# Performance work log

Hardware: AMD Instinct MI355X
Metric: run time of the kernel (lower is better)

Reference implementation:

```python
import jax, jax.numpy as jnp
import numpy as np

DIM = 512
HEADS = 8
DHEAD = DIM // 8          # 64
INNER = HEADS * DHEAD     # 512
M = DIM // 2              # 256 landmarks
ITERS = 6                 # pinv iterations
SCALE = DHEAD ** -0.5
LN_EPS = 1e-5             # torch LayerNorm default
KCONV = 33                # residual_conv_kernel default


def setup_inputs() -> dict:
    key = jax.random.key(0)
    ks = jax.random.split(key, 5)
    B, N = 2, 4096
    x = jax.random.normal(ks[0], (B, N, DIM), jnp.float32)
    ln_w = jnp.ones((DIM,), jnp.float32)
    ln_b = jnp.zeros((DIM,), jnp.float32)
    qkv_w = jax.random.normal(ks[1], (3 * INNER, DIM), jnp.float32) * 0.02
    out_w = jax.random.normal(ks[2], (DIM, INNER), jnp.float32) * 0.02
    out_b = jnp.zeros((DIM,), jnp.float32)
    conv_w = jax.random.normal(ks[3], (HEADS, 1, KCONV, 1), jnp.float32) * 0.05
    return dict(x=x, ln_w=ln_w, ln_b=ln_b, qkv_w=qkv_w,
                out_w=out_w, out_b=out_b, conv_w=conv_w)


def moore_penrose_pinv(x, iters=ITERS):
    # faithful to lucidrains: global (scalar) max over row/col abs-sums
    abs_x = jnp.abs(x)
    z = jnp.swapaxes(x, -1, -2) / (jnp.max(abs_x.sum(-1)) * jnp.max(abs_x.sum(-2)))
    I = jnp.eye(x.shape[-1], dtype=x.dtype)
    for _ in range(iters):
        xz = x @ z
        z = 0.25 * z @ (13 * I - xz @ (15 * I - xz @ (7 * I - xz)))
    return z


def reference(x, ln_w, ln_b, qkv_w, out_w, out_b, conv_w):
    B, N, D = x.shape
    # LayerNorm
    mu = x.mean(-1, keepdims=True)
    var = ((x - mu) ** 2).mean(-1, keepdims=True)
    xn = (x - mu) / jnp.sqrt(var + LN_EPS) * ln_w + ln_b
    # qkv projection (N divisible by M -> no padding branch)
    qkv = xn @ qkv_w.T                                   # [B,N,3*INNER]
    q, k, v = jnp.split(qkv, 3, axis=-1)

    def to_heads(t):
        return t.reshape(B, N, HEADS, DHEAD).transpose(0, 2, 1, 3)  # [B,H,N,Dh]

    q, k, v = to_heads(q), to_heads(k), to_heads(v)
    q = q * SCALE
    l = N // M  # tokens per landmark
    q_land = q.reshape(B, HEADS, M, l, DHEAD).mean(3)    # [B,H,M,Dh]
    k_land = k.reshape(B, HEADS, M, l, DHEAD).mean(3)
    sim1 = jnp.einsum('bhid,bhjd->bhij', q, k_land)      # [B,H,N,M]
    sim2 = jnp.einsum('bhid,bhjd->bhij', q_land, k_land) # [B,H,M,M]
    sim3 = jnp.einsum('bhid,bhjd->bhij', q_land, k)      # [B,H,M,N]
    a1 = jax.nn.softmax(sim1, -1)
    a2 = jax.nn.softmax(sim2, -1)
    a3 = jax.nn.softmax(sim3, -1)
    a2_inv = moore_penrose_pinv(a2)
    out = (a1 @ a2_inv) @ (a3 @ v)                       # [B,H,N,Dh]
    # depthwise residual conv on v along sequence (kernel 33, pad 16)
    res = jax.lax.conv_general_dilated(
        v, conv_w, window_strides=(1, 1),
        padding=((KCONV // 2, KCONV // 2), (0, 0)),
        dimension_numbers=('NCHW', 'OIHW', 'NCHW'),
        feature_group_count=HEADS)
    out = out + res
    out = out.transpose(0, 2, 1, 3).reshape(B, N, INNER)
    attn_out = out @ out_w.T + out_b                     # dropout = eval identity
    return x + attn_out
```

## Files before the change

kernel.cpp:

```cpp
#include <hip/hip_runtime.h>
#include <math.h>

#define DIMD  512
#define NSEQ  4096
#define BATCH 2
#define HEADS 8
#define DHEAD 64
#define MLAND 256
#define BH    (BATCH*HEADS)
#define QSCALE 0.125f
#define LN_EPS 1e-5f
#define KCONV 33

typedef __attribute__((ext_vector_type(8))) short bf16x8;
typedef __attribute__((ext_vector_type(4))) float f32x4;

#define WB(p, mb) ((char*)(p) + (size_t)(mb) * 1048576ull)

__device__ __forceinline__ unsigned short f2b(float f) {
  unsigned u = __float_as_uint(f);
  return (unsigned short)((u + 0x7FFFu + ((u >> 16) & 1u)) >> 16);
}
__device__ __forceinline__ float b2f(unsigned short h) {
  return __uint_as_float(((unsigned)h) << 16);
}

__device__ __forceinline__ float block_red(float v, float* s4, bool sum) {
#pragma unroll
  for (int o = 32; o; o >>= 1) {
    float t = __shfl_xor(v, o);
    v = sum ? v + t : fmaxf(v, t);
  }
  int wid = threadIdx.x >> 6;
  if ((threadIdx.x & 63) == 0) s4[wid] = v;
  __syncthreads();
  float r = sum ? (s4[0] + s4[1] + s4[2] + s4[3])
                : fmaxf(fmaxf(s4[0], s4[1]), fmaxf(s4[2], s4[3]));
  __syncthreads();
  return r;
}

__device__ __forceinline__ void gload16(const unsigned short* g, short* lds) {
  __builtin_amdgcn_global_load_lds(
      (const __attribute__((address_space(1))) void*)g,
      (__attribute__((address_space(3))) void*)lds, 16, 0, 0);
}

template<int ROWS>
__device__ __forceinline__ void stage_lds(const unsigned short* __restrict__ g, int ld,
                                          short* lds, int tid) {
  int l = tid & 63, w = tid >> 6;
  int r_in = l >> 2, c8 = (l & 3) * 8;
  constexpr int PER = ROWS / 64;
#pragma unroll
  for (int p = 0; p < PER; ++p) {
    int r0 = (w * PER + p) * 16;
    gload16(g + (size_t)(r0 + r_in) * ld + c8, lds + r0 * 32);
  }
}

__device__ __forceinline__ void mma_step32(const short* As, const short* Bs,
                                           int wrow, int wcol, int l, f32x4 acc[4][4]) {
  int lr = l & 15, lk = (l >> 4) * 8;
  bf16x8 af[4], bf_[4];
#pragma unroll
  for (int f = 0; f < 4; ++f) {
    af[f]  = *(const bf16x8*)&As[(wrow + f * 16 + lr) * 32 + lk];
    bf_[f] = *(const bf16x8*)&Bs[(wcol + f * 16 + lr) * 32 + lk];
  }
#pragma unroll
  for (int i = 0; i < 4; ++i)
#pragma unroll
    for (int j = 0; j < 4; ++j)
      acc[i][j] = __builtin_amdgcn_mfma_f32_16x16x32_bf16(af[i], bf_[j], acc[i][j], 0, 0, 0);
}


__global__ void k_init(unsigned* scal) {
  if (threadIdx.x < 4) scal[threadIdx.x] = 0u;
}

__global__ __launch_bounds__(256) void k_ln(const float* __restrict__ x,
                                            const float* __restrict__ w,
                                            const float* __restrict__ b,
                                            unsigned short* __restrict__ xnh) {
  int lane = threadIdx.x & 63;
  int row = blockIdx.x * 4 + (threadIdx.x >> 6);
  const float* xr = x + (size_t)row * DIMD;
  float4 v0 = *(const float4*)&xr[lane * 8];
  float4 v1 = *(const float4*)&xr[lane * 8 + 4];
  float s  = v0.x + v0.y + v0.z + v0.w + v1.x + v1.y + v1.z + v1.w;
  float ss = v0.x*v0.x + v0.y*v0.y + v0.z*v0.z + v0.w*v0.w
           + v1.x*v1.x + v1.y*v1.y + v1.z*v1.z + v1.w*v1.w;
#pragma unroll
  for (int o = 32; o; o >>= 1) { s += __shfl_xor(s, o); ss += __shfl_xor(ss, o); }
  float mu = s * (1.f / 512.f);
  float var = ss * (1.f / 512.f) - mu * mu;
  float rstd = rsqrtf(var + LN_EPS);
  float4 w0 = *(const float4*)&w[lane * 8];
  float4 w1 = *(const float4*)&w[lane * 8 + 4];
  float4 b0 = *(const float4*)&b[lane * 8];
  float4 b1 = *(const float4*)&b[lane * 8 + 4];
  float o0x = (v0.x - mu) * rstd * w0.x + b0.x;
  float o0y = (v0.y - mu) * rstd * w0.y + b0.y;
  float o0z = (v0.z - mu) * rstd * w0.z + b0.z;
  float o0w = (v0.w - mu) * rstd * w0.w + b0.w;
  float o1x = (v1.x - mu) * rstd * w1.x + b1.x;
  float o1y = (v1.y - mu) * rstd * w1.y + b1.y;
  float o1z = (v1.z - mu) * rstd * w1.z + b1.z;
  float o1w = (v1.w - mu) * rstd * w1.w + b1.w;
  uint4 pk;
  pk.x = (unsigned)f2b(o0x) | ((unsigned)f2b(o0y) << 16);
  pk.y = (unsigned)f2b(o0z) | ((unsigned)f2b(o0w) << 16);
  pk.z = (unsigned)f2b(o1x) | ((unsigned)f2b(o1y) << 16);
  pk.w = (unsigned)f2b(o1z) | ((unsigned)f2b(o1w) << 16);
  *(uint4*)&xnh[(size_t)row * DIMD + lane * 8] = pk;
}

__global__ __launch_bounds__(256) void k_wconv(const float* __restrict__ qkvw,
                                               const float* __restrict__ outw,
                                               unsigned short* __restrict__ wqh,
                                               unsigned short* __restrict__ owh) {
  int idx = blockIdx.x * 256 + threadIdx.x;
  if (idx < 786432) wqh[idx] = f2b(qkvw[idx]);
  else owh[idx - 786432] = f2b(outw[idx - 786432]);
}

__global__ __launch_bounds__(256) void k_qkv_mfma(const unsigned short* __restrict__ xnh,
                                                  const unsigned short* __restrict__ wqh,
                                                  unsigned short* __restrict__ qh,
                                                  unsigned short* __restrict__ kh,
                                                  unsigned short* __restrict__ vh,
                                                  unsigned short* __restrict__ vTh) {
  __shared__ short As[128 * 32], Bs[128 * 32];
  int tid = threadIdx.x, l = tid & 63, wid = tid >> 6;
  int wrow = (wid >> 1) * 64, wcol = (wid & 1) * 64;
  int m0 = blockIdx.y * 128, c0 = blockIdx.x * 128;
  f32x4 acc[4][4] = {};
  for (int k0 = 0; k0 < 512; k0 += 32) {
    __syncthreads();
    stage_lds<128>(xnh + (size_t)m0 * 512 + k0, 512, As, tid);
    stage_lds<128>(wqh + (size_t)c0 * 512 + k0, 512, Bs, tid);
    __syncthreads();
    mma_step32(As, Bs, wrow, wcol, l, acc);
  }
  const int which = c0 >> 9;
#pragma unroll
  for (int i = 0; i < 4; ++i) {
#pragma unroll
    for (int j = 0; j < 4; ++j) {
      int col = c0 + wcol + j * 16 + (l & 15);
      int hh = (col >> 6) & 7, d = col & 63;
      int m_base = m0 + wrow + i * 16 + ((l >> 4) * 4);
      int bb = m_base >> 12, n0 = m_base & 4095;
      size_t hb = (size_t)(bb * 8 + hh);
      if (which == 0) {
#pragma unroll
        for (int r = 0; r < 4; ++r)
          qh[(hb * 4096 + n0 + r) * 64 + d] = f2b(acc[i][j][r] * QSCALE);
      } else if (which == 1) {
#pragma unroll
        for (int r = 0; r < 4; ++r)
          kh[(hb * 4096 + n0 + r) * 64 + d] = f2b(acc[i][j][r]);
      } else {
        ushort4 hv;
        hv.x = f2b(acc[i][j][0]); hv.y = f2b(acc[i][j][1]);
        hv.z = f2b(acc[i][j][2]); hv.w = f2b(acc[i][j][3]);
#pragma unroll
        for (int r = 0; r < 4; ++r)
          vh[(hb * 4096 + n0 + r) * 64 + d] = (&hv.x)[r];
        *(ushort4*)&vTh[(hb * 64 + d) * 4096 + n0] = hv;
      }
    }
  }
}

__global__ __launch_bounds__(256) void k_land(const unsigned short* __restrict__ q,
                                              const unsigned short* __restrict__ k,
                                              float* __restrict__ ql,
                                              float* __restrict__ kl,
                                              unsigned short* __restrict__ qlh,
                                              unsigned short* __restrict__ klh) {
  int idx = blockIdx.x * 256 + threadIdx.x;
  int sel = idx >= (BH * MLAND * DHEAD);
  int e = sel ? idx - BH * MLAND * DHEAD : idx;
  int bh = e >> 14; int m = (e >> 6) & 255; int d = e & 63;
  const unsigned short* src = sel ? k : q;
  size_t base = ((size_t)bh * 4096 + m * 16) * 64 + d;
  float s = 0;
#pragma unroll
  for (int t = 0; t < 16; ++t) s += b2f(src[base + t * 64]);
  float val = s * (1.f / 16.f);
  (sel ? kl : ql)[e] = val;
  (sel ? klh : qlh)[e] = f2b(val);
}

__global__ __launch_bounds__(256) void k_sim2(const float* __restrict__ ql,
                                              const float* __restrict__ kl,
                                              float* __restrict__ a2,
                                              unsigned short* __restrict__ a2h) {
  __shared__ float qs[64];
  __shared__ float s4[4];
  int i = blockIdx.x, bh = blockIdx.y, tid = threadIdx.x;
  if (tid < 16) ((float4*)qs)[tid] = ((const float4*)(ql + ((size_t)bh * 256 + i) * 64))[tid];
  __syncthreads();
  const float* kr = kl + ((size_t)bh * 256 + tid) * 64;
  float s = 0;
#pragma unroll
  for (int d = 0; d < 64; d += 4) {
    float4 kv = *(const float4*)&kr[d];
    s += qs[d] * kv.x + qs[d + 1] * kv.y + qs[d + 2] * kv.z + qs[d + 3] * kv.w;
  }
  float mx = block_red(s, s4, false);
  float p = expf(s - mx);
  float tot = block_red(p, s4, true);
  float val = p / tot;
  a2[((size_t)bh * 256 + i) * 256 + tid] = val;
  a2h[((size_t)bh * 256 + i) * 256 + tid] = f2b(val);
}

__global__ __launch_bounds__(256) void k_pinv_red(const float* __restrict__ a2,
                                                  unsigned* __restrict__ scal) {
  __shared__ float s4[4];
  int bh = blockIdx.x, tid = threadIdx.x;
  const float* m = a2 + (size_t)bh * 65536;
  float cs = 0;
  for (int i = 0; i < 256; ++i) cs += fabsf(m[(size_t)i * 256 + tid]);
  float rs = 0;
  const float* row = m + (size_t)tid * 256;
  for (int j = 0; j < 256; j += 4) {
    float4 v = *(const float4*)&row[j];
    rs += fabsf(v.x) + fabsf(v.y) + fabsf(v.z) + fabsf(v.w);
  }
  float mc = block_red(cs, s4, false);
  float mr = block_red(rs, s4, false);
  if (tid == 0) {
    atomicMax(&scal[0], __float_as_uint(mr));
    atomicMax(&scal[1], __float_as_uint(mc));
  }
}

__global__ __launch_bounds__(256) void k_z0h(const float* __restrict__ a2,
                                             const unsigned* __restrict__ scal,
                                             unsigned short* __restrict__ zh,
                                             unsigned short* __restrict__ zTh) {
  int idx = blockIdx.x * 256 + threadIdx.x;
  float inv = 1.f / (__uint_as_float(scal[0]) * __uint_as_float(scal[1]));
  int bh = idx >> 16, r = (idx >> 8) & 255, c = idx & 255;
  zh[idx]  = f2b(a2[((size_t)bh << 16) + (c << 8) + r] * inv);
  zTh[idx] = f2b(a2[idx] * inv);
}

__global__ __launch_bounds__(256) void k_pg2(const unsigned short* __restrict__ A,
                                             const unsigned short* __restrict__ Bsrc,
                                             unsigned short* __restrict__ C,
                                             unsigned short* __restrict__ CT,
                                             float g, float bI, float s) {
  __shared__ short As[8 * 64 * 32], Bs[8 * 64 * 32];
  int tid = threadIdx.x, l = tid & 63, w = tid >> 6;
  int i0 = blockIdx.y * 64, j0 = blockIdx.x * 64;
  int bh = blockIdx.z;
  A += (size_t)bh * 65536; Bsrc += (size_t)bh * 65536;

#pragma unroll
  for (int ks = 0; ks < 8; ++ks)
    stage_lds<64>(A + (size_t)i0 * 256 + ks * 32, 256, As + ks * 2048, tid);

#pragma unroll
  for (int u = tid; u < 2048; u += 256) {
    int r = u >> 5, q8 = u & 31;
    int ks = q8 >> 2, p = q8 & 3;
    uint4 vv = *(const uint4*)(Bsrc + (size_t)(j0 + r) * 256 + q8 * 8);
    unsigned short* e = (unsigned short*)&vv;
    int n = j0 + r, kb = q8 * 8;
#pragma unroll
    for (int q = 0; q < 8; ++q) {
      float f = b2f(e[q]) * g + ((n == kb + q) ? bI : 0.f);
      e[q] = f2b(f);
    }
    *(uint4*)(Bs + ks * 2048 + r * 32 + p * 8) = vv;
  }
  __syncthreads();

  int lr = l & 15, lk = (l >> 4) * 8;
  f32x4 acc[4] = {};
#pragma unroll
  for (int ks = 0; ks < 8; ++ks) {
    const short* Ac = As + ks * 2048;
    const short* Bc = Bs + ks * 2048;
    bf16x8 af = *(const bf16x8*)&Ac[(w * 16 + lr) * 32 + lk];
#pragma unroll
    for (int j = 0; j < 4; ++j) {
      bf16x8 bf_ = *(const bf16x8*)&Bc[(j * 16 + lr) * 32 + lk];
      acc[j] = __builtin_amdgcn_mfma_f32_16x16x32_bf16(af, bf_, acc[j], 0, 0, 0);
    }
  }

#pragma unroll
  for (int j = 0; j < 4; ++j) {
    int col = j0 + j * 16 + lr;
    int row0 = i0 + w * 16 + (l >> 4) * 4;
    ushort4 hv;
    hv.x = f2b(acc[j][0] * s); hv.y = f2b(acc[j][1] * s);
    hv.z = f2b(acc[j][2] * s); hv.w = f2b(acc[j][3] * s);
    if (CT) *(ushort4*)&CT[(size_t)bh * 65536 + (size_t)col * 256 + row0] = hv;
    if (C) {
      unsigned short* cb = C + (size_t)bh * 65536 + (size_t)row0 * 256 + col;
      cb[0] = hv.x; cb[256] = hv.y; cb[512] = hv.z; cb[768] = hv.w;
    }
  }
}

__global__ __launch_bounds__(256) void k_sim3_mfma(const unsigned short* __restrict__ qlh,
                                                   const unsigned short* __restrict__ kh,
                                                   unsigned short* __restrict__ sim3h) {
  __shared__ short As[128 * 32], Bs[128 * 32];
  int tid = threadIdx.x, l = tid & 63, wid = tid >> 6;
  int wrow = (wid >> 1) * 64, wcol = (wid & 1) * 64;
  int bh = blockIdx.z;
  int m0 = blockIdx.y * 128, n0 = blockIdx.x * 128;
  const unsigned short* A = qlh + (size_t)bh * 256 * 64;
  const unsigned short* B = kh + (size_t)bh * 4096 * 64;
  f32x4 acc[4][4] = {};
  for (int k0 = 0; k0 < 64; k0 += 32) {
    __syncthreads();
    stage_lds<128>(A + (size_t)m0 * 64 + k0, 64, As, tid);
    stage_lds<128>(B + (size_t)n0 * 64 + k0, 64, Bs, tid);
    __syncthreads();
    mma_step32(As, Bs, wrow, wcol, l, acc);
  }
  unsigned short* Cm = sim3h + (size_t)bh * 1048576;
#pragma unroll
  for (int i = 0; i < 4; ++i)
#pragma unroll
    for (int j = 0; j < 4; ++j) {
      int col = n0 + wcol + j * 16 + (l & 15);
      int row0 = m0 + wrow + i * 16 + (l >> 4) * 4;
#pragma unroll
      for (int r = 0; r < 4; ++r)
        Cm[(size_t)(row0 + r) * 4096 + col] = f2b(acc[i][j][r]);
    }
}

__global__ __launch_bounds__(256) void k_sm4096h(unsigned short* __restrict__ sim) {
  __shared__ float s4[4];
  int m = blockIdx.x, bh = blockIdx.y, tid = threadIdx.x;
  unsigned short* row = sim + ((size_t)bh * 256 + m) * 4096;
  float v[16];
  float mx = -1e30f;
#pragma unroll
  for (int i = 0; i < 16; ++i) { v[i] = b2f(row[i * 256 + tid]); mx = fmaxf(mx, v[i]); }
  mx = block_red(mx, s4, false);
  float ssum = 0;
#pragma unroll
  for (int i = 0; i < 16; ++i) { v[i] = expf(v[i] - mx); ssum += v[i]; }
  ssum = block_red(ssum, s4, true);
  float inv = 1.f / ssum;
#pragma unroll
  for (int i = 0; i < 16; ++i) row[i * 256 + tid] = f2b(v[i] * inv);
}

__global__ __launch_bounds__(256) void k_a3v_mfma(const unsigned short* __restrict__ a3h,
                                                  const unsigned short* __restrict__ vTh,
                                                  float* __restrict__ part) {
  __shared__ short As[256 * 32], Bs[64 * 32];
  int tid = threadIdx.x, l = tid & 63, wid = tid >> 6;
  int wrow = wid * 64, wcol = 0;
  int kc = blockIdx.x, bh = blockIdx.z;
  const unsigned short* A = a3h + (size_t)bh * 1048576 + kc * 512;
  const unsigned short* B = vTh + (size_t)bh * 262144 + kc * 512;
  f32x4 acc[4][4] = {};
  for (int k0 = 0; k0 < 512; k0 += 32) {
    __syncthreads();
    stage_lds<256>(A + k0, 4096, As, tid);
    stage_lds<64>(B + k0, 4096, Bs, tid);
    __syncthreads();
    mma_step32(As, Bs, wrow, wcol, l, acc);
  }
  float* P = part + ((size_t)(kc * 16 + bh)) * 16384;
#pragma unroll
  for (int i = 0; i < 4; ++i)
#pragma unroll
    for (int j = 0; j < 4; ++j) {
      int col = j * 16 + (l & 15);
      int row0 = wrow + i * 16 + (l >> 4) * 4;
#pragma unroll
      for (int r = 0; r < 4; ++r)
        P[(size_t)(row0 + r) * 64 + col] = acc[i][j][r];
    }
}

__global__ __launch_bounds__(256) void k_a3v_redT(const float* __restrict__ part,
                                                  unsigned short* __restrict__ a3vT) {
  int idx = blockIdx.x * 256 + threadIdx.x;
  int m = idx & 255, d = (idx >> 8) & 63, bh = idx >> 14;
  float s = 0;
#pragma unroll
  for (int c = 0; c < 8; ++c) s += part[((size_t)(c * 16 + bh) * 256 + m) * 64 + d];
  a3vT[idx] = f2b(s);
}

__global__ __launch_bounds__(256) void k_wm_mfma(const unsigned short* __restrict__ zh,
                                                 const unsigned short* __restrict__ a3vTh,
                                                 unsigned short* __restrict__ wmTh) {
  __shared__ short As[256 * 32], Bs[64 * 32];
  int tid = threadIdx.x, l = tid & 63, wid = tid >> 6;
  int wrow = wid * 64, wcol = 0;
  int bh = blockIdx.z;
  const unsigned short* A = zh + (size_t)bh * 65536;
  const unsigned short* B = a3vTh + (size_t)bh * 16384;
  f32x4 acc[4][4] = {};
  for (int k0 = 0; k0 < 256; k0 += 32) {
    __syncthreads();
    stage_lds<256>(A + k0, 256, As, tid);
    stage_lds<64>(B + k0, 256, Bs, tid);
    __syncthreads();
    mma_step32(As, Bs, wrow, wcol, l, acc);
  }
  unsigned short* W = wmTh + (size_t)bh * 16384;
#pragma unroll
  for (int i = 0; i < 4; ++i)
#pragma unroll
    for (int j = 0; j < 4; ++j) {
      int col = j * 16 + (l & 15);
      int row0 = wrow + i * 16 + (l >> 4) * 4;
#pragma unroll
      for (int r = 0; r < 4; ++r)
        W[(size_t)col * 256 + row0 + r] = f2b(acc[i][j][r]);
    }
}

#define FSM_Q    0
#define FSM_KL   16384
#define FSM_WMT  0
#define FSM_P    32768
#define FSM_OUT  0
#define FSM_V    32768
__global__ __launch_bounds__(512) void k_fused_mfma(const unsigned short* __restrict__ qh,
                                                    const unsigned short* __restrict__ klh,
                                                    const unsigned short* __restrict__ wmTh,
                                                    const unsigned short* __restrict__ vh,
                                                    const float* __restrict__ cw,
                                                    unsigned short* __restrict__ yh) {
  __shared__ char sm[55808];
  int tid = threadIdx.x, l = tid & 63, w = tid >> 6;
  int h = blockIdx.y, b = blockIdx.z, bh = b * HEADS + h;
  int n0 = blockIdx.x * 128;
  const char* qg = (const char*)(qh + ((size_t)bh * 4096 + n0) * 64);
  const char* kg = (const char*)(klh + (size_t)bh * 256 * 64);

#pragma unroll
  for (int u = tid; u < 1024; u += 512) {
    int row = u >> 3, cb = (u & 7) * 16;
    *(uint4*)(sm + FSM_Q + row * 128 + (cb ^ ((row & 7) << 4))) =
        *(const uint4*)(qg + row * 128 + cb);
  }
#pragma unroll
  for (int u = tid; u < 2048; u += 512) {
    int row = u >> 3, cb = (u & 7) * 16;
    *(uint4*)(sm + FSM_KL + row * 128 + (cb ^ ((row & 7) << 4))) =
        *(const uint4*)(kg + row * 128 + cb);
  }
  __syncthreads();

  int lr = l & 15, lkb = (l >> 4) * 16;
  int arow = 16 * w + lr;
  int aswz = (arow & 7) << 4;
  f32x4 acc[16] = {};
#pragma unroll
  for (int ks = 0; ks < 2; ++ks) {
    bf16x8 af = *(const bf16x8*)(sm + FSM_Q + arow * 128 + ((ks * 64 + lkb) ^ aswz));
#pragma unroll
    for (int j = 0; j < 16; ++j) {
      int brow = j * 16 + lr;
      bf16x8 bf_ = *(const bf16x8*)(sm + FSM_KL + brow * 128 + ((ks * 64 + lkb) ^ ((brow & 7) << 4)));
      acc[j] = __builtin_amdgcn_mfma_f32_16x16x32_bf16(af, bf_, acc[j], 0, 0, 0);
    }
  }

#pragma unroll
  for (int r = 0; r < 4; ++r) {
    float mx = -1e30f;
#pragma unroll
    for (int j = 0; j < 16; ++j) mx = fmaxf(mx, acc[j][r]);
#pragma unroll
    for (int o = 8; o; o >>= 1) mx = fmaxf(mx, __shfl_xor(mx, o));
    float s = 0.f;
#pragma unroll
    for (int j = 0; j < 16; ++j) { float e = expf(acc[j][r] - mx); acc[j][r] = e; s += e; }
#pragma unroll
    for (int o = 8; o; o >>= 1) s += __shfl_xor(s, o);
    float inv = 1.f / s;
#pragma unroll
    for (int j = 0; j < 16; ++j) acc[j][r] *= inv;
  }
  __syncthreads();

  const char* wg = (const char*)(wmTh + (size_t)bh * 16384);
#pragma unroll
  for (int u = tid; u < 2048; u += 512) {
    int row = u >> 5, cb = (u & 31) * 16;
    *(uint4*)(sm + FSM_WMT + row * 512 + (cb ^ ((row & 7) << 4))) =
        *(const uint4*)(wg + row * 512 + cb);
  }

  f32x4 acc2[4] = {};
  int prow0 = 16 * w + (l >> 4) * 4;
#pragma unroll
  for (int mc = 0; mc < 4; ++mc) {
    __syncthreads();
#pragma unroll
    for (int j2 = 0; j2 < 4; ++j2)
#pragma unroll
      for (int r = 0; r < 4; ++r) {
        int row = prow0 + r;
        int colb = (j2 * 16 + lr) * 2;
        *(unsigned short*)(sm + FSM_P + row * 128 + (colb ^ ((row & 7) << 4))) =
            f2b(acc[mc * 4 + j2][r]);
      }
    __syncthreads();
#pragma unroll
    for (int ks = 0; ks < 2; ++ks) {
      bf16x8 af = *(const bf16x8*)(sm + FSM_P + arow * 128 + ((ks * 64 + lkb) ^ aswz));
#pragma unroll
      for (int j = 0; j < 4; ++j) {
        int brow = j * 16 + lr;
        bf16x8 bf_ = *(const bf16x8*)(sm + FSM_WMT + brow * 512 +
                                      ((mc * 128 + ks * 64 + lkb) ^ ((brow & 7) << 4)));
        acc2[j] = __builtin_amdgcn_mfma_f32_16x16x32_bf16(af, bf_, acc2[j], 0, 0, 0);
      }
    }
  }
  __syncthreads();

#pragma unroll
  for (int j = 0; j < 4; ++j)
#pragma unroll
    for (int r = 0; r < 4; ++r)
      *(float*)(sm + FSM_OUT + (prow0 + r) * 256 + (j * 16 + lr) * 4) = acc2[j][r];

  const char* vg = (const char*)(vh + (size_t)bh * 4096 * 64);
#pragma unroll
  for (int u = tid; u < 1280; u += 512) {
    int row = u >> 3, cb = (u & 7) * 16;
    int n = n0 - 16 + row;
    uint4 vv; vv.x = 0; vv.y = 0; vv.z = 0; vv.w = 0;
    if (n >= 0 && n < 4096) vv = *(const uint4*)(vg + (size_t)n * 128 + cb);
    *(uint4*)(sm + FSM_V + row * 144 + cb) = vv;
  }
  __syncthreads();

#pragma unroll
  for (int u = tid; u < 1024; u += 512) {
    int row = u >> 3, d8 = (u & 7) * 8;
    float r8[8] = {};
#pragma unroll 1
    for (int t = 0; t < KCONV; ++t) {
      float wt = cw[h * KCONV + t];
      ushort4 a0 = *(const ushort4*)(sm + FSM_V + (row + t) * 144 + d8 * 2);
      ushort4 a1 = *(const ushort4*)(sm + FSM_V + (row + t) * 144 + d8 * 2 + 8);
      r8[0] += wt * b2f(a0.x); r8[1] += wt * b2f(a0.y);
      r8[2] += wt * b2f(a0.z); r8[3] += wt * b2f(a0.w);
      r8[4] += wt * b2f(a1.x); r8[5] += wt * b2f(a1.y);
      r8[6] += wt * b2f(a1.z); r8[7] += wt * b2f(a1.w);
    }
    const float* ol = (const float*)(sm + FSM_OUT + row * 256 + d8 * 4);
    ushort4 s0, s1;
    s0.x = f2b(r8[0] + ol[0]); s0.y = f2b(r8[1] + ol[1]);
    s0.z = f2b(r8[2] + ol[2]); s0.w = f2b(r8[3] + ol[3]);
    s1.x = f2b(r8[4] + ol[4]); s1.y = f2b(r8[5] + ol[5]);
    s1.z = f2b(r8[6] + ol[6]); s1.w = f2b(r8[7] + ol[7]);
    unsigned short* yp = yh + ((size_t)b * 4096 + n0 + row) * 512 + h * 64 + d8;
    *(ushort4*)yp = s0;
    *(ushort4*)(yp + 4) = s1;
  }
}

__global__ __launch_bounds__(256) void k_outproj_mfma(const unsigned short* __restrict__ yh,
                                                      const unsigned short* __restrict__ owh,
                                                      const float* __restrict__ bias,
                                                      const float* __restrict__ x,
                                                      float* __restrict__ out) {
  __shared__ short As[128 * 32], Bs[128 * 32];
  int tid = threadIdx.x, l = tid & 63, wid = tid >> 6;
  int wrow = (wid >> 1) * 64, wcol = (wid & 1) * 64;
  int m0 = blockIdx.y * 128, c0 = blockIdx.x * 128;
  f32x4 acc[4][4] = {};
  for (int k0 = 0; k0 < 512; k0 += 32) {
    __syncthreads();
    stage_lds<128>(yh + (size_t)m0 * 512 + k0, 512, As, tid);
    stage_lds<128>(owh + (size_t)c0 * 512 + k0, 512, Bs, tid);
    __syncthreads();
    mma_step32(As, Bs, wrow, wcol, l, acc);
  }
#pragma unroll
  for (int i = 0; i < 4; ++i)
#pragma unroll
    for (int j = 0; j < 4; ++j) {
      int col = c0 + wcol + j * 16 + (l & 15);
      int row0 = m0 + wrow + i * 16 + (l >> 4) * 4;
      float bb = bias[col];
#pragma unroll
      for (int r = 0; r < 4; ++r) {
        size_t o = (size_t)(row0 + r) * 512 + col;
        out[o] = acc[i][j][r] + x[o] + bb;
      }
    }
}

extern "C" void kernel_launch(void* const* d_in, const int* in_sizes, int n_in,
                              void* d_out, int out_size, void* d_ws, size_t ws_size,
                              hipStream_t stream) {
  const float* x      = (const float*)d_in[0];
  const float* ln_w   = (const float*)d_in[1];
  const float* ln_b   = (const float*)d_in[2];
  const float* qkv_w  = (const float*)d_in[3];
  const float* out_w  = (const float*)d_in[4];
  const float* out_b  = (const float*)d_in[5];
  const float* conv_w = (const float*)d_in[6];
  float* out = (float*)d_out;

  unsigned short* vh  = (unsigned short*)WB(d_ws, 0);
  float* ql   = (float*)WB(d_ws, 48);
  float* kl   = (float*)WB(d_ws, 49);
  float* a2   = (float*)WB(d_ws, 50);
  float* part = (float*)WB(d_ws, 54);
  unsigned* scal = (unsigned*)WB(d_ws, 63);
  unsigned short* xnh  = (unsigned short*)WB(d_ws, 64);
  unsigned short* wqh  = (unsigned short*)WB(d_ws, 72);
  unsigned short* owh  = (unsigned short*)WB(d_ws, 74);
  unsigned short* kh   = (unsigned short*)WB(d_ws, 76);
  unsigned short* vTh  = (unsigned short*)WB(d_ws, 84);
  unsigned short* qlh  = (unsigned short*)WB(d_ws, 92);
  unsigned short* a2h  = (unsigned short*)WB(d_ws, 93);
  unsigned short* zA   = (unsigned short*)WB(d_ws, 95);
  unsigned short* zAT  = (unsigned short*)WB(d_ws, 97);
  unsigned short* zB   = (unsigned short*)WB(d_ws, 99);
  unsigned short* zBT  = (unsigned short*)WB(d_ws, 101);
  unsigned short* Am   = (unsigned short*)WB(d_ws, 103);
  unsigned short* AmT  = (unsigned short*)WB(d_ws, 105);
  unsigned short* W2T  = (unsigned short*)WB(d_ws, 107);
  unsigned short* W4T  = (unsigned short*)WB(d_ws, 109);
  unsigned short* sim3h= (unsigned short*)WB(d_ws, 111);
  unsigned short* a3vTh= (unsigned short*)WB(d_ws, 143);
  unsigned short* yh   = (unsigned short*)WB(d_ws, 144);
  unsigned short* qhb  = (unsigned short*)WB(d_ws, 152);
  unsigned short* klhb = (unsigned short*)WB(d_ws, 168);
  unsigned short* wmTh = (unsigned short*)WB(d_ws, 169);

  k_init<<<1, 64, 0, stream>>>(scal);
  k_ln<<<2048, 256, 0, stream>>>(x, ln_w, ln_b, xnh);
  k_wconv<<<4096, 256, 0, stream>>>(qkv_w, out_w, wqh, owh);
  k_qkv_mfma<<<dim3(12, 64), 256, 0, stream>>>(xnh, wqh, qhb, kh, vh, vTh);
  k_land<<<2048, 256, 0, stream>>>(qhb, kh, ql, kl, qlh, klhb);
  k_sim2<<<dim3(256, 16), 256, 0, stream>>>(ql, kl, a2, a2h);
  k_pinv_red<<<16, 256, 0, stream>>>(a2, scal);
  k_z0h<<<4096, 256, 0, stream>>>(a2, scal, zA, zAT);

  unsigned short *zc = zA, *zcT = zAT, *zn = zB, *znT = zBT;
  dim3 gpg(4, 4, 16);
  for (int it = 0; it < 6; ++it) {
    k_pg2<<<gpg, 256, 0, stream>>>(a2h, zcT, Am, AmT, 1.f, 0.f, 1.f);
    k_pg2<<<gpg, 256, 0, stream>>>(Am, AmT, (unsigned short*)nullptr, W2T, -1.f, 7.f, 1.f);
    k_pg2<<<gpg, 256, 0, stream>>>(Am, W2T, (unsigned short*)nullptr, W4T, -1.f, 15.f, 1.f);
    k_pg2<<<gpg, 256, 0, stream>>>(zc, W4T, zn, znT, -1.f, 13.f, 0.25f);
    unsigned short* t;
    t = zc; zc = zn; zn = t;
    t = zcT; zcT = znT; znT = t;
  }

  k_sim3_mfma<<<dim3(32, 2, 16), 256, 0, stream>>>(qlh, kh, sim3h);
  k_sm4096h<<<dim3(256, 16), 256, 0, stream>>>(sim3h);
  k_a3v_mfma<<<dim3(8, 1, 16), 256, 0, stream>>>(sim3h, vTh, part);
  k_a3v_redT<<<1024, 256, 0, stream>>>(part, a3vTh);
  k_wm_mfma<<<dim3(1, 1, 16), 256, 0, stream>>>(zA, a3vTh, wmTh);
  k_fused_mfma<<<dim3(32, 8, 2), 512, 0, stream>>>(qhb, klhb, wmTh, vh, conv_w, yh);
  k_outproj_mfma<<<dim3(4, 64), 256, 0, stream>>>(yh, owh, out_b, x, out);
}
```

Before: 368.8 us.

## Fuse softmax normalization into a3v staging, merge LN with weight conversion

The sim3 softmax kernel now only computes per-row max and reciprocal sum, and the a3v GEMM applies exp and normalization while staging its A tile. This removes the full bf16 write-back of the 16x256x4096 softmax matrix. LayerNorm and weight conversion become a single launch, and the pinv GEMM grid is flattened so the batch-head index varies fastest. The trade-off is extra exp work inside the a3v GEMM staging loop, on a small 128-block grid.

After: 357.4 us. -3.1%, faster.

```diff
diff --git a/kernel.cpp b/kernel.cpp
--- a/kernel.cpp
+++ b/kernel.cpp
@@ -80,10 +80,20 @@
   if (threadIdx.x < 4) scal[threadIdx.x] = 0u;
 }
 
-__global__ __launch_bounds__(256) void k_ln(const float* __restrict__ x,
-                                            const float* __restrict__ w,
-                                            const float* __restrict__ b,
-                                            unsigned short* __restrict__ xnh) {
+__global__ __launch_bounds__(256) void k_ln_wconv(const float* __restrict__ x,
+                                                  const float* __restrict__ w,
+                                                  const float* __restrict__ b,
+                                                  const float* __restrict__ qkvw,
+                                                  const float* __restrict__ outw,
+                                                  unsigned short* __restrict__ xnh,
+                                                  unsigned short* __restrict__ wqh,
+                                                  unsigned short* __restrict__ owh) {
+  if (blockIdx.x >= 2048) {
+    int idx = (blockIdx.x - 2048) * 256 + threadIdx.x;
+    if (idx < 786432) wqh[idx] = f2b(qkvw[idx]);
+    else owh[idx - 786432] = f2b(outw[idx - 786432]);
+    return;
+  }
   int lane = threadIdx.x & 63;
   int row = blockIdx.x * 4 + (threadIdx.x >> 6);
   const float* xr = x + (size_t)row * DIMD;
@@ -117,15 +127,6 @@
   *(uint4*)&xnh[(size_t)row * DIMD + lane * 8] = pk;
 }
 
-__global__ __launch_bounds__(256) void k_wconv(const float* __restrict__ qkvw,
-                                               const float* __restrict__ outw,
-                                               unsigned short* __restrict__ wqh,
-                                               unsigned short* __restrict__ owh) {
-  int idx = blockIdx.x * 256 + threadIdx.x;
-  if (idx < 786432) wqh[idx] = f2b(qkvw[idx]);
-  else owh[idx - 786432] = f2b(outw[idx - 786432]);
-}
-
 __global__ __launch_bounds__(256) void k_qkv_mfma(const unsigned short* __restrict__ xnh,
                                                   const unsigned short* __restrict__ wqh,
                                                   unsigned short* __restrict__ qh,
@@ -258,8 +259,8 @@
                                              float g, float bI, float s) {
   __shared__ short As[8 * 64 * 32], Bs[8 * 64 * 32];
   int tid = threadIdx.x, l = tid & 63, w = tid >> 6;
-  int i0 = blockIdx.y * 64, j0 = blockIdx.x * 64;
-  int bh = blockIdx.z;
+  int bh = blockIdx.x & 15, t = blockIdx.x >> 4;
+  int i0 = (t >> 2) * 64, j0 = (t & 3) * 64;
   A += (size_t)bh * 65536; Bsrc += (size_t)bh * 65536;
 
 #pragma unroll
@@ -342,10 +343,11 @@
     }
 }
 
-__global__ __launch_bounds__(256) void k_sm4096h(unsigned short* __restrict__ sim) {
+__global__ __launch_bounds__(256) void k_rowstat(const unsigned short* __restrict__ sim,
+                                                 float* __restrict__ rs) {
   __shared__ float s4[4];
   int m = blockIdx.x, bh = blockIdx.y, tid = threadIdx.x;
-  unsigned short* row = sim + ((size_t)bh * 256 + m) * 4096;
+  const unsigned short* row = sim + ((size_t)bh * 256 + m) * 4096;
   float v[16];
   float mx = -1e30f;
 #pragma unroll
@@ -353,15 +355,17 @@
   mx = block_red(mx, s4, false);
   float ssum = 0;
 #pragma unroll
-  for (int i = 0; i < 16; ++i) { v[i] = expf(v[i] - mx); ssum += v[i]; }
+  for (int i = 0; i < 16; ++i) ssum += expf(v[i] - mx);
   ssum = block_red(ssum, s4, true);
-  float inv = 1.f / ssum;
-#pragma unroll
-  for (int i = 0; i < 16; ++i) row[i * 256 + tid] = f2b(v[i] * inv);
+  if (tid == 0) {
+    rs[(size_t)(bh * 256 + m) * 2]     = mx;
+    rs[(size_t)(bh * 256 + m) * 2 + 1] = 1.f / ssum;
+  }
 }
 
 __global__ __launch_bounds__(256) void k_a3v_mfma(const unsigned short* __restrict__ a3h,
                                                   const unsigned short* __restrict__ vTh,
+                                                  const float* __restrict__ rs,
                                                   float* __restrict__ part) {
   __shared__ short As[256 * 32], Bs[64 * 32];
   int tid = threadIdx.x, l = tid & 63, wid = tid >> 6;
@@ -369,10 +373,21 @@
   int kc = blockIdx.x, bh = blockIdx.z;
   const unsigned short* A = a3h + (size_t)bh * 1048576 + kc * 512;
   const unsigned short* B = vTh + (size_t)bh * 262144 + kc * 512;
+  rs += (size_t)bh * 512;
   f32x4 acc[4][4] = {};
   for (int k0 = 0; k0 < 512; k0 += 32) {
     __syncthreads();
-    stage_lds<256>(A + k0, 4096, As, tid);
+#pragma unroll
+    for (int u = tid; u < 1024; u += 256) {
+      int r = u >> 2, c = u & 3;
+      uint4 vv = *(const uint4*)(A + (size_t)r * 4096 + k0 + c * 8);
+      unsigned short* e = (unsigned short*)&vv;
+      float m_ = rs[r * 2], inv_ = rs[r * 2 + 1];
+#pragma unroll
+      for (int q = 0; q < 8; ++q)
+        e[q] = f2b(expf(b2f(e[q]) - m_) * inv_);
+      *(uint4*)(As + r * 32 + c * 8) = vv;
+    }
     stage_lds<64>(B + k0, 4096, Bs, tid);
     __syncthreads();
     mma_step32(As, Bs, wrow, wcol, l, acc);
@@ -625,6 +640,7 @@
   float* kl   = (float*)WB(d_ws, 49);
   float* a2   = (float*)WB(d_ws, 50);
   float* part = (float*)WB(d_ws, 54);
+  float* rs   = (float*)WB(d_ws, 62);
   unsigned* scal = (unsigned*)WB(d_ws, 63);
   unsigned short* xnh  = (unsigned short*)WB(d_ws, 64);
   unsigned short* wqh  = (unsigned short*)WB(d_ws, 72);
@@ -649,8 +665,7 @@
   unsigned short* wmTh = (unsigned short*)WB(d_ws, 169);
 
   k_init<<<1, 64, 0, stream>>>(scal);
-  k_ln<<<2048, 256, 0, stream>>>(x, ln_w, ln_b, xnh);
-  k_wconv<<<4096, 256, 0, stream>>>(qkv_w, out_w, wqh, owh);
+  k_ln_wconv<<<6144, 256, 0, stream>>>(x, ln_w, ln_b, qkv_w, out_w, xnh, wqh, owh);
   k_qkv_mfma<<<dim3(12, 64), 256, 0, stream>>>(xnh, wqh, qhb, kh, vh, vTh);
   k_land<<<2048, 256, 0, stream>>>(qhb, kh, ql, kl, qlh, klhb);
   k_sim2<<<dim3(256, 16), 256, 0, stream>>>(ql, kl, a2, a2h);
@@ -658,20 +673,19 @@
   k_z0h<<<4096, 256, 0, stream>>>(a2, scal, zA, zAT);
 
   unsigned short *zc = zA, *zcT = zAT, *zn = zB, *znT = zBT;
-  dim3 gpg(4, 4, 16);
   for (int it = 0; it < 6; ++it) {
-    k_pg2<<<gpg, 256, 0, stream>>>(a2h, zcT, Am, AmT, 1.f, 0.f, 1.f);
-    k_pg2<<<gpg, 256, 0, stream>>>(Am, AmT, (unsigned short*)nullptr, W2T, -1.f, 7.f, 1.f);
-    k_pg2<<<gpg, 256, 0, stream>>>(Am, W2T, (unsigned short*)nullptr, W4T, -1.f, 15.f, 1.f);
-    k_pg2<<<gpg, 256, 0, stream>>>(zc, W4T, zn, znT, -1.f, 13.f, 0.25f);
+    k_pg2<<<256, 256, 0, stream>>>(a2h, zcT, Am, AmT, 1.f, 0.f, 1.f);
+    k_pg2<<<256, 256, 0, stream>>>(Am, AmT, (unsigned short*)nullptr, W2T, -1.f, 7.f, 1.f);
+    k_pg2<<<256, 256, 0, stream>>>(Am, W2T, (unsigned short*)nullptr, W4T, -1.f, 15.f, 1.f);
+    k_pg2<<<256, 256, 0, stream>>>(zc, W4T, zn, znT, -1.f, 13.f, 0.25f);
     unsigned short* t;
     t = zc; zc = zn; zn = t;
     t = zcT; zcT = znT; znT = t;
   }
 
   k_sim3_mfma<<<dim3(32, 2, 16), 256, 0, stream>>>(qlh, kh, sim3h);
-  k_sm4096h<<<dim3(256, 16), 256, 0, stream>>>(sim3h);
-  k_a3v_mfma<<<dim3(8, 1, 16), 256, 0, stream>>>(sim3h, vTh, part);
+  k_rowstat<<<dim3(256, 16), 256, 0, stream>>>(sim3h, rs);
+  k_a3v_mfma<<<dim3(8, 1, 16), 256, 0, stream>>>(sim3h, vTh, rs, part);
   k_a3v_redT<<<1024, 256, 0, stream>>>(part, a3vTh);
   k_wm_mfma<<<dim3(1, 1, 16), 256, 0, stream>>>(zA, a3vTh, wmTh);
   k_fused_mfma<<<dim3(32, 8, 2), 512, 0, stream>>>(qhb, klhb, wmTh, vh, conv_w, yh);
```
